# Performance work log

Measured on AMD Instinct MI355X. Metric: run time of the kernel, lower is better.

## Reference

```python
import jax, jax.numpy as jnp
import numpy as np

PATCH = 3
ALPHA = 0.1

def unfold_patches(f, p):
    # Emulates F.unfold with zero padding p//2, stride 1: [B,C,H,W] -> [B, C*p*p, H, W].
    # Descriptor-dim ordering differs from torch's, but the correlation sum over the
    # descriptor dim is permutation-invariant, so the output is identical.
    pad = p // 2
    B, C, H, W = f.shape
    fp = jnp.pad(f, ((0, 0), (0, 0), (pad, pad), (pad, pad)))
    patches = [fp[:, :, i:i + H, j:j + W] for i in range(p) for j in range(p)]
    return jnp.concatenate(patches, axis=1)


def setup_inputs() -> dict:
    key = jax.random.key(0)
    k1, k2 = jax.random.split(key)
    x_rgb = jax.random.uniform(k1, (4, 3, 64, 64), dtype=jnp.float32)
    feature = jax.random.normal(k2, (4, 64, 64, 64), dtype=jnp.float32)
    return {"x_rgb": x_rgb, "feature": feature}


def reference(x_rgb, feature):
    B, _, H, W = x_rgb.shape
    HW = H * W
    rgb = x_rgb.reshape(B, 3, HW).transpose(0, 2, 1)            # [B, HW, 3]
    local = unfold_patches(feature, PATCH).reshape(B, -1, HW)    # [B, D, HW], D = C*p*p
    # correlation = K^T K over descriptor dim -> [B, HW, HW]
    corr = jnp.einsum('bdp,bdq->bpq', local, local)
    attn = jax.nn.softmax(corr / ALPHA, axis=-1)
    weighted = jnp.einsum('bpq,bqc->bpc', attn, rgb)             # [B, HW, 3]
    return weighted.transpose(0, 2, 1).reshape(B, 3, H, W)
```

## Files before the change

kernel.cpp:

```cpp
#include <hip/hip_runtime.h>
#include <hip/hip_bf16.h>

typedef __attribute__((ext_vector_type(4))) float f32x4;
typedef __attribute__((ext_vector_type(2))) long long l64x2;

constexpr int kB = 4, kC = 64, kH = 64, kW = 64;
constexpr int kHW = kH * kW;
constexpr int kD  = kC * 9;
constexpr int KSPLIT = 8;
constexpr int KBLK = 32;
constexpr int QWAVE = 32;
constexpr int QWG = 256;
constexpr int NTILE = kHW / KSPLIT / KBLK;
constexpr int ROWB8 = 640;
constexpr int TILEB = KBLK * ROWB8;
constexpr int TCHUNK = TILEB / 16;

#define FSCALE 3.79828370f
#define SEED_SLACK 8.0f

__global__ __launch_bounds__(256)
void nlwa_unfold(const float* __restrict__ feat, unsigned char* __restrict__ Kd) {
    int idx = blockIdx.x * 256 + threadIdx.x;
    if (idx >= kB * kHW * (ROWB8 / 8)) return;
    int piece = idx % (ROWB8 / 8);
    int v = (idx / (ROWB8 / 8)) % kHW;
    int b = idx / ((ROWB8 / 8) * kHW);
    unsigned long long pack = 0ULL;
    if (piece < 72) {
        int y0 = v >> 6, x0 = v & 63;
        #pragma unroll
        for (int j = 0; j < 8; ++j) {
            int d = piece * 8 + j;
            int c = d / 9, dl = d % 9;
            int y = y0 + dl / 3 - 1;
            int x = x0 + dl % 3 - 1;
            float val = 0.f;
            if ((unsigned)y < 64u && (unsigned)x < 64u)
                val = feat[((b * kC + c) * kH + y) * kW + x] * FSCALE;
            unsigned int fb = __builtin_bit_cast(unsigned int, val * 0x1p-120f);
            unsigned int mag = ((fb & 0x7fffffffu) + 0x80000u) >> 20;
            if (mag > 0x7eu) mag = 0x7eu;
            unsigned long long u8 = ((fb >> 31) << 7) | mag;
            pack |= u8 << (8 * j);
        }
    }
    int c = (piece >> 3) * 4 + (piece & 3);
    int half = (piece >> 2) & 1;
    int cp = c ^ (v & 7);
    *(unsigned long long*)(Kd + (size_t)(b * kHW + v) * ROWB8 + cp * 16 + half * 8) = pack;
}

__global__ __launch_bounds__(512, 2)
void nlwa_attn(const unsigned char* __restrict__ Kd,
               const float* __restrict__ rgb,
               float* __restrict__ part) {
    __shared__ alignas(16) unsigned char Ks[2][KBLK][ROWB8];

    int orig = blockIdx.x;
    int wg = (orig & 7) * 64 + (orig >> 3);
    int qblk = wg & 15;
    int pr = wg >> 4;
    int ks = pr & 7;
    int b  = pr >> 3;

    int tid = threadIdx.x, lane = tid & 63, wid = tid >> 6;
    int lr = lane & 15, lg = lane >> 4;
    int s7 = lr & 7;
    int qwave = qblk * QWG + wid * QWAVE;
    int k0 = ks * (kHW / KSPLIT);

    int4 qb[2][9];
    #pragma unroll
    for (int g = 0; g < 2; ++g) {
        const unsigned char* qbase = Kd + (size_t)(b * kHW + qwave + g * 16 + lr) * ROWB8;
        #pragma unroll
        for (int p = 0; p < 9; ++p)
            qb[g][p] = *(const int4*)(qbase + (((p * 4 + lg) ^ s7) << 4));
    }

    float m[2], l[2] = {0.f, 0.f};
    float O[2][3] = {{0,0,0},{0,0,0}};
    #pragma unroll
    for (int g = 0; g < 2; ++g) {
        float ss = 0.f;
        #pragma unroll
        for (int p = 0; p < 9; ++p) {
            const int* w4 = (const int*)&qb[g][p];
            #pragma unroll
            for (int j = 0; j < 4; ++j) {
                unsigned int w32 = (unsigned int)w4[j];
                #pragma unroll
                for (int byi = 0; byi < 4; ++byi) {
                    unsigned int mag = (w32 >> (8 * byi)) & 0x7fu;
                    float v = __builtin_bit_cast(float, mag << 20) * 0x1p120f;
                    ss = fmaf(v, v, ss);
                }
            }
        }
        ss += __shfl_xor(ss, 16);
        ss += __shfl_xor(ss, 32);
        m[g] = ss - SEED_SLACK;
    }

    const unsigned char* ksrc = Kd + (size_t)(b * kHW + k0) * ROWB8;
    unsigned char* lds0 = &Ks[0][0][0];

    auto stage = [&](int t, int bufi) {
        const unsigned char* src = ksrc + (size_t)t * TILEB;
        unsigned char* dstb = lds0 + bufi * TILEB;
        #pragma unroll
        for (int it = 0; it < 3; ++it) {
            int base = it * 512 + wid * 64;
            if (base < TCHUNK) {
                __builtin_amdgcn_global_load_lds(
                    (const __attribute__((address_space(1))) void*)(src + (size_t)(base + lane) * 16),
                    (__attribute__((address_space(3))) void*)(dstb + (size_t)base * 16),
                    16, 0, 0);
            }
        }
    };

    stage(0, 0);
    __syncthreads();

    int lo2 = s7 & 3, h = s7 >> 2;
    int r0 = lr * ROWB8 + ((lg ^ lo2) << 4);
    int e0 = r0 + h * 64, o0 = r0 - h * 64;

    int buf = 0;
    for (int t = 0; t < NTILE; ++t) {
        if (t + 1 < NTILE) stage(t + 1, buf ^ 1);

        const unsigned char* kb = lds0 + buf * TILEB;
        f32x4 acc[2][2];
        #pragma unroll
        for (int g = 0; g < 2; ++g) {
            acc[g][0] = (f32x4){0.f, 0.f, 0.f, 0.f};
            acc[g][1] = (f32x4){0.f, 0.f, 0.f, 0.f};
        }

        #pragma unroll
        for (int p = 0; p < 9; ++p) {
            int off = ((p & 1) ? o0 : e0) + p * 64;
            int4 ka = *(const int4*)(kb + off);
            int4 kc = *(const int4*)(kb + 16 * ROWB8 + off);
            l64x2 ka64 = __builtin_bit_cast(l64x2, ka);
            l64x2 kc64 = __builtin_bit_cast(l64x2, kc);
            #pragma unroll
            for (int w01 = 0; w01 < 2; ++w01) {
                long long a0 = ka64[w01], a1 = kc64[w01];
                #pragma unroll
                for (int g = 0; g < 2; ++g) {
                    long long bq = __builtin_bit_cast(l64x2, qb[g][p])[w01];
                    acc[g][0] = __builtin_amdgcn_mfma_f32_16x16x32_fp8_fp8(a0, bq, acc[g][0], 0, 0, 0);
                    acc[g][1] = __builtin_amdgcn_mfma_f32_16x16x32_fp8_fp8(a1, bq, acc[g][1], 0, 0, 0);
                }
            }
        }

        float pm[2];
        #pragma unroll
        for (int g = 0; g < 2; ++g)
            pm[g] = fmaxf(
                fmaxf(fmaxf(acc[g][0][0], acc[g][0][1]), fmaxf(acc[g][0][2], acc[g][0][3])),
                fmaxf(fmaxf(acc[g][1][0], acc[g][1][1]), fmaxf(acc[g][1][2], acc[g][1][3])));

        float dmx = fmaxf(pm[0] - m[0], pm[1] - m[1]);
        if (__any(dmx >= -25.f)) {
            int kt0 = k0 + t * KBLK;
            #pragma unroll
            for (int g = 0; g < 2; ++g) {
                float v = pm[g];
                v = fmaxf(v, __shfl_xor(v, 16));
                v = fmaxf(v, __shfl_xor(v, 32));
                float mn = fmaxf(m[g], v);
                float al = exp2f(m[g] - mn);
                m[g] = mn;
                l[g] *= al;
                O[g][0] *= al; O[g][1] *= al; O[g][2] *= al;
            }
            float4 rv[2][3];
            #pragma unroll
            for (int s = 0; s < 2; ++s)
                #pragma unroll
                for (int c = 0; c < 3; ++c)
                    rv[s][c] = *(const float4*)(rgb + (size_t)(b * 3 + c) * kHW + kt0 + s * 16 + lg * 4);
            #pragma unroll
            for (int g = 0; g < 2; ++g) {
                #pragma unroll
                for (int s = 0; s < 2; ++s) {
                    float p0 = exp2f(acc[g][s][0] - m[g]);
                    float p1 = exp2f(acc[g][s][1] - m[g]);
                    float p2 = exp2f(acc[g][s][2] - m[g]);
                    float p3 = exp2f(acc[g][s][3] - m[g]);
                    l[g] += p0 + p1 + p2 + p3;
                    #pragma unroll
                    for (int c = 0; c < 3; ++c)
                        O[g][c] += p0 * rv[s][c].x + p1 * rv[s][c].y
                                 + p2 * rv[s][c].z + p3 * rv[s][c].w;
                }
            }
        }
        __syncthreads();
        buf ^= 1;
    }

    #pragma unroll
    for (int g = 0; g < 2; ++g) {
        l[g] += __shfl_xor(l[g], 16); l[g] += __shfl_xor(l[g], 32);
        #pragma unroll
        for (int c = 0; c < 3; ++c) {
            O[g][c] += __shfl_xor(O[g][c], 16);
            O[g][c] += __shfl_xor(O[g][c], 32);
        }
    }
    if (lg == 0) {
        #pragma unroll
        for (int g = 0; g < 2; ++g) {
            int q = qwave + g * 16 + lr;
            float* p = part + ((size_t)(b * kHW + q) * KSPLIT + ks) * 5;
            p[0] = m[g]; p[1] = l[g]; p[2] = O[g][0]; p[3] = O[g][1]; p[4] = O[g][2];
        }
    }
}

__global__ __launch_bounds__(256)
void nlwa_merge(const float* __restrict__ part, float* __restrict__ out) {
    int idx = blockIdx.x * 256 + threadIdx.x;
    if (idx >= kB * kHW) return;
    int b = idx >> 12, q = idx & 4095;
    const float* p = part + (size_t)idx * KSPLIT * 5;
    float M = -INFINITY;
    #pragma unroll
    for (int s = 0; s < KSPLIT; ++s) M = fmaxf(M, p[s * 5]);
    float L = 0.f, o0 = 0.f, o1 = 0.f, o2 = 0.f;
    #pragma unroll
    for (int s = 0; s < KSPLIT; ++s) {
        float a = exp2f(p[s * 5] - M);
        L  += p[s * 5 + 1] * a;
        o0 += p[s * 5 + 2] * a;
        o1 += p[s * 5 + 3] * a;
        o2 += p[s * 5 + 4] * a;
    }
    float inv = 1.f / L;
    out[(b * 3 + 0) * kHW + q] = o0 * inv;
    out[(b * 3 + 1) * kHW + q] = o1 * inv;
    out[(b * 3 + 2) * kHW + q] = o2 * inv;
}

__global__ __launch_bounds__(64)
void nlwa_naive(const float* __restrict__ feat, const float* __restrict__ rgb,
                float* __restrict__ out) {
    int p = blockIdx.x, b = blockIdx.y;
    int pi = p >> 6, pj = p & 63;
    int t = threadIdx.x;
    __shared__ float pdesc[kD];
    __shared__ float rows[kC][3][kW];
    __shared__ float red[64][5];

    for (int d = t; d < kD; d += 64) {
        int c = d / 9, dl = d % 9;
        int y = pi + dl / 3 - 1, x = pj + dl % 3 - 1;
        pdesc[d] = ((unsigned)y < 64u && (unsigned)x < 64u)
                 ? feat[((b * kC + c) * kH + y) * kW + x] : 0.f;
    }
    float m = -INFINITY, l = 0.f, O0 = 0.f, O1 = 0.f, O2 = 0.f;
    for (int qi = 0; qi < kH; ++qi) {
        __syncthreads();
        for (int f = t; f < kC * 3 * kW; f += 64) {
            int x = f & 63, yy = (f >> 6) % 3, c = f / (3 * kW);
            int y = qi + yy - 1;
            rows[c][yy][x] = ((unsigned)y < 64u) ? feat[((b * kC + c) * kH + y) * kW + x] : 0.f;
        }
        __syncthreads();
        float s = 0.f;
        for (int c = 0; c < kC; ++c)
            for (int dl = 0; dl < 9; ++dl) {
                int x = t + dl % 3 - 1;
                float fv = ((unsigned)x < 64u) ? rows[c][dl / 3][x] : 0.f;
                s += pdesc[c * 9 + dl] * fv;
            }
        s *= 14.4269504089f;
        int q = qi * 64 + t;
        float mn = fmaxf(m, s);
        float al = exp2f(m - mn);
        float pv = exp2f(s - mn);
        l = l * al + pv;
        O0 = O0 * al + pv * rgb[(b * 3 + 0) * kHW + q];
        O1 = O1 * al + pv * rgb[(b * 3 + 1) * kHW + q];
        O2 = O2 * al + pv * rgb[(b * 3 + 2) * kHW + q];
        m = mn;
    }
    red[t][0] = m; red[t][1] = l; red[t][2] = O0; red[t][3] = O1; red[t][4] = O2;
    __syncthreads();
    if (t == 0) {
        float M = -INFINITY;
        for (int i = 0; i < 64; ++i) M = fmaxf(M, red[i][0]);
        float L = 0, A = 0, Bv = 0, Cv = 0;
        for (int i = 0; i < 64; ++i) {
            float a = exp2f(red[i][0] - M);
            L += red[i][1] * a; A += red[i][2] * a; Bv += red[i][3] * a; Cv += red[i][4] * a;
        }
        out[(b * 3 + 0) * kHW + p] = A / L;
        out[(b * 3 + 1) * kHW + p] = Bv / L;
        out[(b * 3 + 2) * kHW + p] = Cv / L;
    }
}

extern "C" void kernel_launch(void* const* d_in, const int* in_sizes, int n_in,
                              void* d_out, int out_size, void* d_ws, size_t ws_size,
                              hipStream_t stream) {
    const float* x_rgb   = (const float*)d_in[0];
    const float* feature = (const float*)d_in[1];
    float* out = (float*)d_out;

    size_t needK = (size_t)kB * kHW * ROWB8;
    size_t needP = (size_t)kB * kHW * KSPLIT * 5 * 4;
    if (ws_size >= needK + needP) {
        unsigned char* Kd = (unsigned char*)d_ws;
        float* partb = (float*)((char*)d_ws + needK);
        int pieces = kB * kHW * (ROWB8 / 8);
        nlwa_unfold<<<(pieces + 255) / 256, 256, 0, stream>>>(feature, Kd);
        nlwa_attn<<<kB * (kHW / QWG) * KSPLIT, 512, 0, stream>>>(Kd, x_rgb, partb);
        nlwa_merge<<<(kB * kHW + 255) / 256, 256, 0, stream>>>(partb, out);
    } else {
        nlwa_naive<<<dim3(kHW, kB), 64, 0, stream>>>(feature, x_rgb, out);
    }
}
```

Before: 92.83 us.

## Triple-buffer key tiles with vmcnt waits, smaller workgroups, and stage rgb in LDS

Workgroups shrink from 512 to 256 threads, each covering 128 queries, and key tiles drop to 16 rows. Tiles now rotate through a triple-buffered LDS ring, prefetched two ahead, with explicit vmcnt waits and a raw barrier in place of __syncthreads. The rgb slice for the key split is loaded into LDS once up front, so the inner loop no longer issues global rgb loads. This aims to hide global latency and raise occupancy, but it doubles the loop trip count and the per-tile barrier and softmax-rescale overhead, and it relies on hand-counted vmcnt values being correct.

```diff
diff --git a/kernel.cpp b/kernel.cpp
--- a/kernel.cpp
+++ b/kernel.cpp
@@ -3,18 +3,24 @@
 
 typedef __attribute__((ext_vector_type(4))) float f32x4;
 typedef __attribute__((ext_vector_type(2))) long long l64x2;
+
+#define AS1 const __attribute__((address_space(1))) void*
+#define AS3 __attribute__((address_space(3))) void*
 
 constexpr int kB = 4, kC = 64, kH = 64, kW = 64;
 constexpr int kHW = kH * kW;
 constexpr int kD  = kC * 9;
 constexpr int KSPLIT = 8;
-constexpr int KBLK = 32;
+constexpr int KBLK = 16;
 constexpr int QWAVE = 32;
-constexpr int QWG = 256;
+constexpr int QWG = 128;
 constexpr int NTILE = kHW / KSPLIT / KBLK;
 constexpr int ROWB8 = 640;
 constexpr int TILEB = KBLK * ROWB8;
 constexpr int TCHUNK = TILEB / 16;
+constexpr int NBUF = 3;
+constexpr int RGB_OFF = NBUF * TILEB;
+constexpr int SMEM_BYTES = RGB_OFF + 3 * 512 * 4;
 
 #define FSCALE 3.79828370f
 #define SEED_SLACK 8.0f
@@ -51,16 +57,16 @@
     *(unsigned long long*)(Kd + (size_t)(b * kHW + v) * ROWB8 + cp * 16 + half * 8) = pack;
 }
 
-__global__ __launch_bounds__(512, 2)
+__global__ __launch_bounds__(256, 4)
 void nlwa_attn(const unsigned char* __restrict__ Kd,
                const float* __restrict__ rgb,
                float* __restrict__ part) {
-    __shared__ alignas(16) unsigned char Ks[2][KBLK][ROWB8];
+    __shared__ alignas(16) unsigned char SM[SMEM_BYTES];
 
     int orig = blockIdx.x;
-    int wg = (orig & 7) * 64 + (orig >> 3);
-    int qblk = wg & 15;
-    int pr = wg >> 4;
+    int wg = (orig & 7) * 128 + (orig >> 3);
+    int qblk = wg & 31;
+    int pr = wg >> 5;
     int ks = pr & 7;
     int b  = pr >> 3;
 
@@ -78,6 +84,40 @@
         for (int p = 0; p < 9; ++p)
             qb[g][p] = *(const int4*)(qbase + (((p * 4 + lg) ^ s7) << 4));
     }
+
+    unsigned char* lds0 = &SM[0];
+    const unsigned char* ksrc = Kd + (size_t)(b * kHW + k0) * ROWB8;
+
+    {
+        int base0 = wid * 64;
+        int ch0 = base0 + lane;
+        __builtin_amdgcn_global_load_lds(
+            (AS1)(rgb + (size_t)(b * 3 + (ch0 >> 7)) * kHW + k0 + ((ch0 & 127) << 2)),
+            (AS3)(lds0 + RGB_OFF + (size_t)base0 * 16), 16, 0, 0);
+        int base1 = 256 + wid * 32;
+        if (lane < 32) {
+            int ch1 = base1 + lane;
+            __builtin_amdgcn_global_load_lds(
+                (AS1)(rgb + (size_t)(b * 3 + (ch1 >> 7)) * kHW + k0 + ((ch1 & 127) << 2)),
+                (AS3)(lds0 + RGB_OFF + (size_t)base1 * 16), 16, 0, 0);
+        }
+    }
+
+    auto stage = [&](int t, int bufi) {
+        const unsigned char* src = ksrc + (size_t)t * TILEB;
+        unsigned char* dstb = lds0 + bufi * TILEB;
+        int base = wid * 160;
+        __builtin_amdgcn_global_load_lds(
+            (AS1)(src + (size_t)(base + lane) * 16), (AS3)(dstb + (size_t)base * 16), 16, 0, 0);
+        __builtin_amdgcn_global_load_lds(
+            (AS1)(src + (size_t)(base + 64 + lane) * 16), (AS3)(dstb + (size_t)(base + 64) * 16), 16, 0, 0);
+        if (lane < 32)
+            __builtin_amdgcn_global_load_lds(
+                (AS1)(src + (size_t)(base + 128 + lane) * 16), (AS3)(dstb + (size_t)(base + 128) * 16), 16, 0, 0);
+    };
+
+    stage(0, 0);
+    stage(1, 1);
 
     float m[2], l[2] = {0.f, 0.f};
     float O[2][3] = {{0,0,0},{0,0,0}};
@@ -103,58 +143,36 @@
         m[g] = ss - SEED_SLACK;
     }
 
-    const unsigned char* ksrc = Kd + (size_t)(b * kHW + k0) * ROWB8;
-    unsigned char* lds0 = &Ks[0][0][0];
-
-    auto stage = [&](int t, int bufi) {
-        const unsigned char* src = ksrc + (size_t)t * TILEB;
-        unsigned char* dstb = lds0 + bufi * TILEB;
-        #pragma unroll
-        for (int it = 0; it < 3; ++it) {
-            int base = it * 512 + wid * 64;
-            if (base < TCHUNK) {
-                __builtin_amdgcn_global_load_lds(
-                    (const __attribute__((address_space(1))) void*)(src + (size_t)(base + lane) * 16),
-                    (__attribute__((address_space(3))) void*)(dstb + (size_t)base * 16),
-                    16, 0, 0);
-            }
-        }
-    };
-
-    stage(0, 0);
-    __syncthreads();
-
     int lo2 = s7 & 3, h = s7 >> 2;
     int r0 = lr * ROWB8 + ((lg ^ lo2) << 4);
     int e0 = r0 + h * 64, o0 = r0 - h * 64;
 
-    int buf = 0;
     for (int t = 0; t < NTILE; ++t) {
-        if (t + 1 < NTILE) stage(t + 1, buf ^ 1);
-
-        const unsigned char* kb = lds0 + buf * TILEB;
-        f32x4 acc[2][2];
-        #pragma unroll
-        for (int g = 0; g < 2; ++g) {
-            acc[g][0] = (f32x4){0.f, 0.f, 0.f, 0.f};
-            acc[g][1] = (f32x4){0.f, 0.f, 0.f, 0.f};
-        }
+        if (t + 1 < NTILE) {
+            asm volatile("s_waitcnt vmcnt(3)" ::: "memory");
+        } else {
+            asm volatile("s_waitcnt vmcnt(0)" ::: "memory");
+        }
+        __builtin_amdgcn_s_barrier();
+        __builtin_amdgcn_sched_barrier(0);
+        if (t + 2 < NTILE) stage(t + 2, (t + 2) % NBUF);
+
+        const unsigned char* kb = lds0 + (t % NBUF) * TILEB;
+        f32x4 acc[2];
+        acc[0] = (f32x4){0.f, 0.f, 0.f, 0.f};
+        acc[1] = (f32x4){0.f, 0.f, 0.f, 0.f};
 
         #pragma unroll
         for (int p = 0; p < 9; ++p) {
-            int off = ((p & 1) ? o0 : e0) + p * 64;
-            int4 ka = *(const int4*)(kb + off);
-            int4 kc = *(const int4*)(kb + 16 * ROWB8 + off);
+            int4 ka = *(const int4*)(kb + ((p & 1) ? o0 : e0) + p * 64);
             l64x2 ka64 = __builtin_bit_cast(l64x2, ka);
-            l64x2 kc64 = __builtin_bit_cast(l64x2, kc);
             #pragma unroll
             for (int w01 = 0; w01 < 2; ++w01) {
-                long long a0 = ka64[w01], a1 = kc64[w01];
+                long long a0 = ka64[w01];
                 #pragma unroll
                 for (int g = 0; g < 2; ++g) {
                     long long bq = __builtin_bit_cast(l64x2, qb[g][p])[w01];
-                    acc[g][0] = __builtin_amdgcn_mfma_f32_16x16x32_fp8_fp8(a0, bq, acc[g][0], 0, 0, 0);
-                    acc[g][1] = __builtin_amdgcn_mfma_f32_16x16x32_fp8_fp8(a1, bq, acc[g][1], 0, 0, 0);
+                    acc[g] = __builtin_amdgcn_mfma_f32_16x16x32_fp8_fp8(a0, bq, acc[g], 0, 0, 0);
                 }
             }
         }
@@ -162,13 +180,10 @@
         float pm[2];
         #pragma unroll
         for (int g = 0; g < 2; ++g)
-            pm[g] = fmaxf(
-                fmaxf(fmaxf(acc[g][0][0], acc[g][0][1]), fmaxf(acc[g][0][2], acc[g][0][3])),
-                fmaxf(fmaxf(acc[g][1][0], acc[g][1][1]), fmaxf(acc[g][1][2], acc[g][1][3])));
+            pm[g] = fmaxf(fmaxf(acc[g][0], acc[g][1]), fmaxf(acc[g][2], acc[g][3]));
 
         float dmx = fmaxf(pm[0] - m[0], pm[1] - m[1]);
         if (__any(dmx >= -25.f)) {
-            int kt0 = k0 + t * KBLK;
             #pragma unroll
             for (int g = 0; g < 2; ++g) {
                 float v = pm[g];
@@ -180,30 +195,23 @@
                 l[g] *= al;
                 O[g][0] *= al; O[g][1] *= al; O[g][2] *= al;
             }
-            float4 rv[2][3];
-            #pragma unroll
-            for (int s = 0; s < 2; ++s)
+            float4 rv[3];
+            #pragma unroll
+            for (int c = 0; c < 3; ++c)
+                rv[c] = *(const float4*)(lds0 + RGB_OFF
+                            + (size_t)((c << 9) + t * KBLK + (lg << 2)) * 4);
+            #pragma unroll
+            for (int g = 0; g < 2; ++g) {
+                float p0 = exp2f(acc[g][0] - m[g]);
+                float p1 = exp2f(acc[g][1] - m[g]);
+                float p2 = exp2f(acc[g][2] - m[g]);
+                float p3 = exp2f(acc[g][3] - m[g]);
+                l[g] += p0 + p1 + p2 + p3;
                 #pragma unroll
                 for (int c = 0; c < 3; ++c)
-                    rv[s][c] = *(const float4*)(rgb + (size_t)(b * 3 + c) * kHW + kt0 + s * 16 + lg * 4);
-            #pragma unroll
-            for (int g = 0; g < 2; ++g) {
-                #pragma unroll
-                for (int s = 0; s < 2; ++s) {
-                    float p0 = exp2f(acc[g][s][0] - m[g]);
-                    float p1 = exp2f(acc[g][s][1] - m[g]);
-                    float p2 = exp2f(acc[g][s][2] - m[g]);
-                    float p3 = exp2f(acc[g][s][3] - m[g]);
-                    l[g] += p0 + p1 + p2 + p3;
-                    #pragma unroll
-                    for (int c = 0; c < 3; ++c)
-                        O[g][c] += p0 * rv[s][c].x + p1 * rv[s][c].y
-                                 + p2 * rv[s][c].z + p3 * rv[s][c].w;
-                }
-            }
-        }
-        __syncthreads();
-        buf ^= 1;
+                    O[g][c] += p0 * rv[c].x + p1 * rv[c].y + p2 * rv[c].z + p3 * rv[c].w;
+            }
+        }
     }
 
     #pragma unroll
@@ -322,7 +330,7 @@
         float* partb = (float*)((char*)d_ws + needK);
         int pieces = kB * kHW * (ROWB8 / 8);
         nlwa_unfold<<<(pieces + 255) / 256, 256, 0, stream>>>(feature, Kd);
-        nlwa_attn<<<kB * (kHW / QWG) * KSPLIT, 512, 0, stream>>>(Kd, x_rgb, partb);
+        nlwa_attn<<<kB * (kHW / QWG) * KSPLIT, 256, 0, stream>>>(Kd, x_rgb, partb);
         nlwa_merge<<<(kB * kHW + 255) / 256, 256, 0, stream>>>(partb, out);
     } else {
         nlwa_naive<<<dim3(kHW, kB), 64, 0, stream>>>(feature, x_rgb, out);
```

Result: no change. 91.83 us (-1.1%).
